# Kernel optimization log

Measured on AMD Instinct MI355X. Metric: run time of the kernel, lower is better.

## Reference

```python
import jax, jax.numpy as jnp
import numpy as np

B, S, H, E, K = 4, 2048, 1024, 8, 2

def setup_inputs() -> dict:
    key = jax.random.key(0)
    k0, k1, k2, k3 = jax.random.split(key, 4)
    x = jax.random.normal(k0, (B, S, H), dtype=jnp.float32)
    # xavier-uniform-like scales
    router_w = jax.random.normal(k1, (E, H), dtype=jnp.float32) * np.float32(1.0 / np.sqrt(H))
    xav1 = np.float32(np.sqrt(2.0 / (2 * H + H)))
    w1 = jax.random.normal(k2, (E, 2 * H, H), dtype=jnp.float32) * xav1
    w2 = jax.random.normal(k3, (E, H, 2 * H), dtype=jnp.float32) * xav1
    return {"x": x, "router_w": router_w, "w1": w1, "w2": w2}

def reference(x, router_w, w1, w2):
    bsz, seq, hidden = x.shape
    n_experts = w1.shape[0]
    tokens = x.reshape(-1, hidden)                      # [T, H]
    T = tokens.shape[0]
    logits = tokens @ router_w.T                        # [T, E]
    topv, topi = jax.lax.top_k(logits, K)               # [T, K]
    w = jax.nn.softmax(topv, axis=-1).astype(tokens.dtype)
    # Dense gate matrix: gate[t, e] = routing weight of expert e for token t
    # (zero for non-selected experts). Equivalent to the torch pad/dispatch/
    # scatter-add combine: padded slots have weight 0 and contribute nothing.
    gate = jnp.zeros((T, n_experts), tokens.dtype).at[jnp.arange(T)[:, None], topi].add(w)
    out = jnp.zeros_like(tokens)
    for e in range(n_experts):  # small fixed expert count
        h = jax.nn.gelu(tokens @ w1[e].T, approximate=False)  # [T, 2H] (torch F.gelu = erf)
        y = h @ w2[e].T                                       # [T, H]
        out = out + gate[:, e:e + 1] * y
    return out.reshape(bsz, seq, hidden)
```

## Files before the change

### kernel.cpp

```cpp
#include <hip/hip_runtime.h>
#include <stdint.h>
#include <math.h>

#define T_TOK 8192
#define H_DIM 1024
#define H2    2048
#define NE    8

typedef unsigned short u16;
typedef __attribute__((ext_vector_type(8))) short bf16x8;
typedef __attribute__((ext_vector_type(4))) float f32x4;

__device__ __forceinline__ u16 f32_to_bf16(float f) {
  union { float f; unsigned u; } c; c.f = f;
  unsigned u = c.u + 0x7fffu + ((c.u >> 16) & 1u);
  return (u16)(u >> 16);
}
__device__ __forceinline__ float bf2f(u16 v) {
  union { unsigned u; float f; } c; c.u = (unsigned)v << 16; return c.f;
}

__device__ __forceinline__ float fast_gelu(float v) {
  float u = v * v;
  float z2 = v * fmaf(u, 0.1029437f, 2.3022078f);
  float e = __builtin_amdgcn_exp2f(z2);
  float r = __builtin_amdgcn_rcpf(1.0f + e);
  return v - v * r;
}

__device__ __forceinline__ void g2l16(const void* g, void* l) {
  __builtin_amdgcn_global_load_lds(
      (const __attribute__((address_space(1))) unsigned*)g,
      (__attribute__((address_space(3))) unsigned*)l, 16, 0, 0);
}

__device__ __forceinline__ int prefix_base(const int* counts, int e) {
  int b = 0;
#pragma unroll
  for (int j = 0; j < NE; j++) b += (j < e) ? counts[j] : 0;
  return b;
}

__global__ __launch_bounds__(256) void prep_kernel(
    const float* __restrict__ x, const float* __restrict__ rw,
    const float* __restrict__ w1, const float* __restrict__ w2,
    u16* __restrict__ xb, u16* __restrict__ w1b, u16* __restrict__ w2b,
    int* __restrict__ tope, float2* __restrict__ gate2,
    int* __restrict__ counts) {
  int blk = blockIdx.x;
  if (blk < T_TOK / 4) {
    int wave = threadIdx.x >> 6;
    int lane = threadIdx.x & 63;
    int t = blk * 4 + wave;
    const float4* x4 = (const float4*)(x + (size_t)t * H_DIM);
    const float4* rw4 = (const float4*)rw;
    u16* xbrow = xb + (size_t)t * H_DIM;

    double acc[NE];
#pragma unroll
    for (int e = 0; e < NE; e++) acc[e] = 0.0;
#pragma unroll
    for (int i = 0; i < 4; i++) {
      int c = lane + 64 * i;
      float4 xv = x4[c];
      ushort4 bv = make_ushort4(f32_to_bf16(xv.x), f32_to_bf16(xv.y),
                                f32_to_bf16(xv.z), f32_to_bf16(xv.w));
      *(ushort4*)(xbrow + c * 4) = bv;
#pragma unroll
      for (int e = 0; e < NE; e++) {
        float4 wv = rw4[e * 256 + c];
        acc[e] += (double)xv.x * wv.x + (double)xv.y * wv.y +
                  (double)xv.z * wv.z + (double)xv.w * wv.w;
      }
    }
#pragma unroll
    for (int off = 32; off >= 1; off >>= 1)
#pragma unroll
      for (int e = 0; e < NE; e++) acc[e] += __shfl_xor(acc[e], off, 64);

    if (lane == 0) {
      int e0 = 0; double v0 = acc[0];
#pragma unroll
      for (int e = 1; e < NE; e++) if (acc[e] > v0) { v0 = acc[e]; e0 = e; }
      int e1 = -1; double v1 = -1e300;
#pragma unroll
      for (int e = 0; e < NE; e++) if (e != e0 && acc[e] > v1) { v1 = acc[e]; e1 = e; }
      double ex = exp(v1 - v0);
      tope[t] = e0 | (e1 << 8);
      gate2[t] = make_float2((float)(1.0 / (1.0 + ex)), (float)(ex / (1.0 + ex)));
    }
  } else {
    int cb = blk - T_TOK / 4;
    if (cb == 0 && threadIdx.x < NE) counts[threadIdx.x] = 0;
    const float* src; u16* dst;
    if (cb < 3072) { src = w1; dst = w1b; }
    else           { src = w2; dst = w2b; cb -= 3072; }
    const int n4 = NE * H2 * H_DIM / 4;
    const int stride = 3072 * 256;
    const float4* s4 = (const float4*)src;
    for (int i = cb * 256 + threadIdx.x; i < n4; i += stride) {
      float4 v = s4[i];
      *(ushort4*)(dst + (size_t)i * 4) = make_ushort4(
          f32_to_bf16(v.x), f32_to_bf16(v.y), f32_to_bf16(v.z), f32_to_bf16(v.w));
    }
  }
}

__global__ __launch_bounds__(256) void build_kernel(
    const int* __restrict__ tope, int* __restrict__ counts,
    int* __restrict__ tok_list, int2* __restrict__ pos2) {
  __shared__ int cts[4][NE];
  __shared__ int gbase[NE];
  int tid = threadIdx.x, lane = tid & 63, w = tid >> 6;
  int t = blockIdx.x * 256 + tid;
  int pk = tope[t];
  int e0 = pk & 0xff, e1 = (pk >> 8) & 0xff;
  unsigned long long lt = ((unsigned long long)1 << lane) - 1;

  int r0 = 0, r1 = 0;
#pragma unroll
  for (int e = 0; e < NE; e++) {
    unsigned long long b0 = __ballot(e0 == e);
    unsigned long long b1 = __ballot(e1 == e);
    int n0 = __popcll(b0), n1 = __popcll(b1);
    if (e0 == e) r0 = __popcll(b0 & lt);
    if (e1 == e) r1 = n0 + __popcll(b1 & lt);
    if (lane == 0) cts[w][e] = n0 + n1;
  }
  __syncthreads();
  if (tid < NE) {
    int bt = cts[0][tid] + cts[1][tid] + cts[2][tid] + cts[3][tid];
    gbase[tid] = atomicAdd(&counts[tid], bt);
  }
  __syncthreads();
  int off0 = gbase[e0] + r0;
  int off1 = gbase[e1] + r1;
#pragma unroll
  for (int wp = 0; wp < 4; wp++) {
    if (wp < w) { off0 += cts[wp][e0]; off1 += cts[wp][e1]; }
  }
  tok_list[e0 * T_TOK + off0] = t;
  tok_list[e1 * T_TOK + off1] = t;
  pos2[t] = make_int2(off0, off1);
}

template <int NKT, int NT, int OUTN, bool GATHER, bool GELU>
__global__ __launch_bounds__(512, 2) void moe_gemm(
    const u16* __restrict__ A, const u16* __restrict__ W,
    u16* __restrict__ O, const int* __restrict__ tok_list,
    const int* __restrict__ counts) {
  int e = blockIdx.x & 7;
  int rem = blockIdx.x >> 3;
  int mt = rem / NT, nt = rem % NT;
  int cnt = counts[e];
  int m0 = mt * 256;
  if (m0 >= cnt) return;
  int base = prefix_base(counts, e);
  const int K = NKT * 64;

  __shared__ u16 lA[2][16384];
  __shared__ u16 lB[2][16384];

  int tid = threadIdx.x;
  int ln = tid & 63, w = tid >> 6;
  int wr = w >> 2, wc = w & 3;
  int quad = ln >> 4, l16 = ln & 15;

  const u16* We = W + (size_t)e * OUTN * K;
  const u16* aptr[4]; const u16* bptr[4];
#pragma unroll
  for (int c = 0; c < 4; ++c) {
    int u = c * 512 + tid;
    int row = u >> 3;
    int chunk = (u & 7) ^ (row & 7);
    int ar = m0 + row; if (ar > cnt - 1) ar = cnt - 1;
    const u16* ab;
    if (GATHER) ab = A + (size_t)tok_list[e * T_TOK + ar] * K;
    else        ab = A + (size_t)(base + ar) * K;
    aptr[c] = ab + chunk * 8;
    bptr[c] = We + (size_t)(nt * 256 + row) * K + chunk * 8;
  }

  int adA[8][2], adB[4][2];
#pragma unroll
  for (int f = 0; f < 8; ++f) {
    int r = wr * 128 + f * 16 + l16;
#pragma unroll
    for (int kk = 0; kk < 2; ++kk)
      adA[f][kk] = r * 64 + ((((kk << 2) | quad) ^ (r & 7)) << 3);
  }
#pragma unroll
  for (int j = 0; j < 4; ++j) {
    int r = wc * 64 + j * 16 + l16;
#pragma unroll
    for (int kk = 0; kk < 2; ++kk)
      adB[j][kk] = r * 64 + ((((kk << 2) | quad) ^ (r & 7)) << 3);
  }

  f32x4 acc[8][4];
#pragma unroll
  for (int i = 0; i < 8; i++)
#pragma unroll
    for (int j = 0; j < 4; j++)
#pragma unroll
      for (int r = 0; r < 4; r++) acc[i][j][r] = 0.f;

#pragma unroll
  for (int c = 0; c < 4; ++c) {
    g2l16(aptr[c], &lA[0][(c * 512 + tid) * 8]);
    g2l16(bptr[c], &lB[0][(c * 512 + tid) * 8]);
  }

#pragma unroll 1
  for (int t = 0; t < NKT; ++t) {
    int d = t & 1;
    asm volatile("s_waitcnt vmcnt(0)" ::: "memory");
    __builtin_amdgcn_s_barrier();
    __builtin_amdgcn_sched_barrier(0);

    const u16* Ab = &lA[d][0];
    const u16* Bb = &lB[d][0];
    bf16x8 af[8], af2[8], bf[4], bf2v[4];
    af[0]  = *(const bf16x8*)(Ab + adA[0][0]);
    af2[0] = *(const bf16x8*)(Ab + adA[0][1]);
#pragma unroll
    for (int j = 0; j < 4; ++j) {
      bf[j]   = *(const bf16x8*)(Bb + adB[j][0]);
      bf2v[j] = *(const bf16x8*)(Bb + adB[j][1]);
    }
#pragma unroll
    for (int f = 1; f < 8; ++f) {
      af[f]  = *(const bf16x8*)(Ab + adA[f][0]);
      af2[f] = *(const bf16x8*)(Ab + adA[f][1]);
    }

    if (t + 1 < NKT) {
#pragma unroll
      for (int c = 0; c < 4; ++c) {
        g2l16(aptr[c] + (t + 1) * 64, &lA[d ^ 1][(c * 512 + tid) * 8]);
        g2l16(bptr[c] + (t + 1) * 64, &lB[d ^ 1][(c * 512 + tid) * 8]);
      }
    }
    __builtin_amdgcn_sched_barrier(0);

    __builtin_amdgcn_s_setprio(1);
#pragma unroll
    for (int mi = 0; mi < 8; ++mi) {
#pragma unroll
      for (int ni = 0; ni < 4; ++ni)
        acc[mi][ni] = __builtin_amdgcn_mfma_f32_16x16x32_bf16(
            af[mi], bf[ni], acc[mi][ni], 0, 0, 0);
#pragma unroll
      for (int ni = 0; ni < 4; ++ni)
        acc[mi][ni] = __builtin_amdgcn_mfma_f32_16x16x32_bf16(
            af2[mi], bf2v[ni], acc[mi][ni], 0, 0, 0);
    }
    __builtin_amdgcn_s_setprio(0);
  }

#pragma unroll
  for (int mi = 0; mi < 8; ++mi) {
    int rb = wr * 128 + mi * 16 + quad * 4;
#pragma unroll
    for (int r = 0; r < 4; ++r) {
      int grow = m0 + rb + r;
      if (grow < cnt) {
        size_t o = (size_t)(base + grow) * OUTN + nt * 256 + wc * 64 + l16;
#pragma unroll
        for (int ni = 0; ni < 4; ++ni) {
          float v = acc[mi][ni][r];
          if (GELU) v = fast_gelu(v);
          O[o + ni * 16] = f32_to_bf16(v);
        }
      }
    }
  }
}

__global__ __launch_bounds__(256) void combine_kernel(
    const u16* __restrict__ y, const int* __restrict__ tope,
    const float2* __restrict__ gate2, const int2* __restrict__ pos2,
    const int* __restrict__ counts, float* __restrict__ out) {
  int t = blockIdx.x;
  int pk = tope[t];
  int e0 = pk & 0xff, e1 = (pk >> 8) & 0xff;
  float2 g = gate2[t];
  int2 p = pos2[t];
  int hb0 = prefix_base(counts, e0);
  int hb1 = prefix_base(counts, e1);
  size_t s0 = (size_t)(hb0 + p.x) * H_DIM + threadIdx.x * 4;
  size_t s1 = (size_t)(hb1 + p.y) * H_DIM + threadIdx.x * 4;
  ushort4 a = *(const ushort4*)(y + s0);
  ushort4 b = *(const ushort4*)(y + s1);
  float4 o;
  o.x = g.x * bf2f(a.x) + g.y * bf2f(b.x);
  o.y = g.x * bf2f(a.y) + g.y * bf2f(b.y);
  o.z = g.x * bf2f(a.z) + g.y * bf2f(b.z);
  o.w = g.x * bf2f(a.w) + g.y * bf2f(b.w);
  *(float4*)(out + (size_t)t * H_DIM + threadIdx.x * 4) = o;
}

extern "C" void kernel_launch(void* const* d_in, const int* in_sizes, int n_in,
                              void* d_out, int out_size, void* d_ws, size_t ws_size,
                              hipStream_t stream) {
  const float* x  = (const float*)d_in[0];
  const float* rw = (const float*)d_in[1];
  const float* w1 = (const float*)d_in[2];
  const float* w2 = (const float*)d_in[3];
  float* out = (float*)d_out;

  char* ws = (char*)d_ws;
  u16* xb       = (u16*)(ws);
  u16* w1b      = (u16*)(ws + 16777216);
  u16* y        = (u16*)(ws + 16777216);
  u16* w2b      = (u16*)(ws + 50331648);
  u16* h        = (u16*)(ws + 83886080);
  int* tok_list = (int*)(ws + 150994944);
  int* tope     = (int*)(ws + 151257088);
  float2* gate2 = (float2*)(ws + 151289856);
  int2* pos2    = (int2*)(ws + 151355392);
  int* counts   = (int*)(ws + 151420928);

  prep_kernel<<<T_TOK / 4 + 6144, 256, 0, stream>>>(x, rw, w1, w2, xb, w1b, w2b,
                                                    tope, gate2, counts);
  build_kernel<<<T_TOK / 256, 256, 0, stream>>>(tope, counts, tok_list, pos2);
  moe_gemm<16, 8, H2, true, true>
      <<<NE * 32 * 8, 512, 0, stream>>>(xb, w1b, h, tok_list, counts);
  moe_gemm<32, 4, H_DIM, false, false>
      <<<NE * 32 * 4, 512, 0, stream>>>(h, w2b, y, tok_list, counts);
  combine_kernel<<<T_TOK, 256, 0, stream>>>(y, tope, gate2, pos2, counts, out);
}
```

Measured before the change: 390.7 us.

## Move w2 bf16 conversion into first expert GEMM and fold w1 conversion into router blocks

The prep kernel no longer has separate weight-conversion blocks. Each router block now also converts a fixed 2048-float4 slice of w1, and the w2 fp32-to-bf16 conversion is done at the start of every block of the first expert GEMM, before its early-exit check, so it overlaps with GEMM work. Launch bounds for moe_gemm drop from 2 to 1 blocks per CU, which allows more registers but lowers occupancy. The aim is to shorten the prep phase and hide the w2 conversion traffic behind compute, at the cost of extra memory traffic inside the GEMM and a possible occupancy loss.

```diff
diff --git a/kernel.cpp b/kernel.cpp
--- a/kernel.cpp
+++ b/kernel.cpp
@@ -43,66 +43,64 @@
 
 __global__ __launch_bounds__(256) void prep_kernel(
     const float* __restrict__ x, const float* __restrict__ rw,
-    const float* __restrict__ w1, const float* __restrict__ w2,
-    u16* __restrict__ xb, u16* __restrict__ w1b, u16* __restrict__ w2b,
+    const float* __restrict__ w1,
+    u16* __restrict__ xb, u16* __restrict__ w1b,
     int* __restrict__ tope, float2* __restrict__ gate2,
     int* __restrict__ counts) {
   int blk = blockIdx.x;
-  if (blk < T_TOK / 4) {
-    int wave = threadIdx.x >> 6;
-    int lane = threadIdx.x & 63;
-    int t = blk * 4 + wave;
-    const float4* x4 = (const float4*)(x + (size_t)t * H_DIM);
-    const float4* rw4 = (const float4*)rw;
-    u16* xbrow = xb + (size_t)t * H_DIM;
-
-    double acc[NE];
-#pragma unroll
-    for (int e = 0; e < NE; e++) acc[e] = 0.0;
-#pragma unroll
-    for (int i = 0; i < 4; i++) {
-      int c = lane + 64 * i;
-      float4 xv = x4[c];
-      ushort4 bv = make_ushort4(f32_to_bf16(xv.x), f32_to_bf16(xv.y),
-                                f32_to_bf16(xv.z), f32_to_bf16(xv.w));
-      *(ushort4*)(xbrow + c * 4) = bv;
-#pragma unroll
-      for (int e = 0; e < NE; e++) {
-        float4 wv = rw4[e * 256 + c];
-        acc[e] += (double)xv.x * wv.x + (double)xv.y * wv.y +
-                  (double)xv.z * wv.z + (double)xv.w * wv.w;
-      }
-    }
-#pragma unroll
-    for (int off = 32; off >= 1; off >>= 1)
-#pragma unroll
-      for (int e = 0; e < NE; e++) acc[e] += __shfl_xor(acc[e], off, 64);
-
-    if (lane == 0) {
-      int e0 = 0; double v0 = acc[0];
-#pragma unroll
-      for (int e = 1; e < NE; e++) if (acc[e] > v0) { v0 = acc[e]; e0 = e; }
-      int e1 = -1; double v1 = -1e300;
-#pragma unroll
-      for (int e = 0; e < NE; e++) if (e != e0 && acc[e] > v1) { v1 = acc[e]; e1 = e; }
-      double ex = exp(v1 - v0);
-      tope[t] = e0 | (e1 << 8);
-      gate2[t] = make_float2((float)(1.0 / (1.0 + ex)), (float)(ex / (1.0 + ex)));
-    }
-  } else {
-    int cb = blk - T_TOK / 4;
-    if (cb == 0 && threadIdx.x < NE) counts[threadIdx.x] = 0;
-    const float* src; u16* dst;
-    if (cb < 3072) { src = w1; dst = w1b; }
-    else           { src = w2; dst = w2b; cb -= 3072; }
-    const int n4 = NE * H2 * H_DIM / 4;
-    const int stride = 3072 * 256;
-    const float4* s4 = (const float4*)src;
-    for (int i = cb * 256 + threadIdx.x; i < n4; i += stride) {
+  if (blk == 0 && threadIdx.x < NE) counts[threadIdx.x] = 0;
+
+  {
+    const float4* s4 = (const float4*)w1;
+    int b0 = blk * 2048 + threadIdx.x;
+#pragma unroll
+    for (int k = 0; k < 8; ++k) {
+      int i = b0 + k * 256;
       float4 v = s4[i];
-      *(ushort4*)(dst + (size_t)i * 4) = make_ushort4(
+      *(ushort4*)(w1b + (size_t)i * 4) = make_ushort4(
           f32_to_bf16(v.x), f32_to_bf16(v.y), f32_to_bf16(v.z), f32_to_bf16(v.w));
     }
+  }
+
+  int wave = threadIdx.x >> 6;
+  int lane = threadIdx.x & 63;
+  int t = blk * 4 + wave;
+  const float4* x4 = (const float4*)(x + (size_t)t * H_DIM);
+  const float4* rw4 = (const float4*)rw;
+  u16* xbrow = xb + (size_t)t * H_DIM;
+
+  double acc[NE];
+#pragma unroll
+  for (int e = 0; e < NE; e++) acc[e] = 0.0;
+#pragma unroll
+  for (int i = 0; i < 4; i++) {
+    int c = lane + 64 * i;
+    float4 xv = x4[c];
+    ushort4 bv = make_ushort4(f32_to_bf16(xv.x), f32_to_bf16(xv.y),
+                              f32_to_bf16(xv.z), f32_to_bf16(xv.w));
+    *(ushort4*)(xbrow + c * 4) = bv;
+#pragma unroll
+    for (int e = 0; e < NE; e++) {
+      float4 wv = rw4[e * 256 + c];
+      acc[e] += (double)xv.x * wv.x + (double)xv.y * wv.y +
+                (double)xv.z * wv.z + (double)xv.w * wv.w;
+    }
+  }
+#pragma unroll
+  for (int off = 32; off >= 1; off >>= 1)
+#pragma unroll
+    for (int e = 0; e < NE; e++) acc[e] += __shfl_xor(acc[e], off, 64);
+
+  if (lane == 0) {
+    int e0 = 0; double v0 = acc[0];
+#pragma unroll
+    for (int e = 1; e < NE; e++) if (acc[e] > v0) { v0 = acc[e]; e0 = e; }
+    int e1 = -1; double v1 = -1e300;
+#pragma unroll
+    for (int e = 0; e < NE; e++) if (e != e0 && acc[e] > v1) { v1 = acc[e]; e1 = e; }
+    double ex = exp(v1 - v0);
+    tope[t] = e0 | (e1 << 8);
+    gate2[t] = make_float2((float)(1.0 / (1.0 + ex)), (float)(ex / (1.0 + ex)));
   }
 }
 
@@ -144,11 +142,23 @@
   pos2[t] = make_int2(off0, off1);
 }
 
-template <int NKT, int NT, int OUTN, bool GATHER, bool GELU>
-__global__ __launch_bounds__(512, 2) void moe_gemm(
+template <int NKT, int NT, int OUTN, bool GATHER, bool GELU, bool CVTW2>
+__global__ __launch_bounds__(512, 1) void moe_gemm(
     const u16* __restrict__ A, const u16* __restrict__ W,
     u16* __restrict__ O, const int* __restrict__ tok_list,
-    const int* __restrict__ counts) {
+    const int* __restrict__ counts,
+    const float* __restrict__ cvt_src, u16* __restrict__ cvt_dst) {
+  if (CVTW2) {
+    const float4* s4 = (const float4*)cvt_src;
+    int b0 = blockIdx.x * 2048 + threadIdx.x;
+#pragma unroll
+    for (int k = 0; k < 4; ++k) {
+      int i = b0 + k * 512;
+      float4 v = s4[i];
+      *(ushort4*)(cvt_dst + (size_t)i * 4) = make_ushort4(
+          f32_to_bf16(v.x), f32_to_bf16(v.y), f32_to_bf16(v.z), f32_to_bf16(v.w));
+    }
+  }
   int e = blockIdx.x & 7;
   int rem = blockIdx.x >> 3;
   int mt = rem / NT, nt = rem % NT;
@@ -321,12 +331,13 @@
   int2* pos2    = (int2*)(ws + 151355392);
   int* counts   = (int*)(ws + 151420928);
 
-  prep_kernel<<<T_TOK / 4 + 6144, 256, 0, stream>>>(x, rw, w1, w2, xb, w1b, w2b,
-                                                    tope, gate2, counts);
+  prep_kernel<<<T_TOK / 4, 256, 0, stream>>>(x, rw, w1, xb, w1b,
+                                             tope, gate2, counts);
   build_kernel<<<T_TOK / 256, 256, 0, stream>>>(tope, counts, tok_list, pos2);
-  moe_gemm<16, 8, H2, true, true>
-      <<<NE * 32 * 8, 512, 0, stream>>>(xb, w1b, h, tok_list, counts);
-  moe_gemm<32, 4, H_DIM, false, false>
-      <<<NE * 32 * 4, 512, 0, stream>>>(h, w2b, y, tok_list, counts);
+  moe_gemm<16, 8, H2, true, true, true>
+      <<<NE * 32 * 8, 512, 0, stream>>>(xb, w1b, h, tok_list, counts, w2, w2b);
+  moe_gemm<32, 4, H_DIM, false, false, false>
+      <<<NE * 32 * 4, 512, 0, stream>>>(h, w2b, y, tok_list, counts,
+                                        nullptr, nullptr);
   combine_kernel<<<T_TOK, 256, 0, stream>>>(y, tope, gate2, pos2, counts, out);
 }
```

After: 378.0 us. 1.03x faster.
